# Kernel optimization log

Measured on AMD Instinct MI355X. Metric: run time of the kernel, lower is better.

The kernel has to match this reference:

```python
import jax, jax.numpy as jnp
import numpy as np

N, E, C, H = 100000, 3200000, 4, 64
EPS = 1e-8


def setup_inputs() -> dict:
    key = jax.random.key(0)
    k1, k2, k3, k4, k5, k6, k7 = jax.random.split(key, 7)
    x = jax.random.uniform(k1, (N, C), dtype=jnp.float32)            # [pm10, u10, v10, aux]
    pos = jax.random.normal(k2, (N, 2), dtype=jnp.float32)           # node coordinates
    edge_index = jax.random.randint(k3, (2, E), 0, N, dtype=jnp.int64)
    # PhysicsFluxLayer edge MLP: in = [x_i, x_j, wind_proj, dist] -> hidden
    fan_in = 2 * C + 2
    mlp_w = jax.random.normal(k4, (H, fan_in), dtype=jnp.float32) / np.sqrt(fan_in)
    mlp_b = jnp.zeros((H,), dtype=jnp.float32)
    # output head (module inits to zero; use small random values for a non-degenerate baseline)
    head_w = jax.random.normal(k5, (1, H), dtype=jnp.float32) * 0.02
    head_b = jax.random.normal(k6, (1,), dtype=jnp.float32) * 0.02
    return {"x": x, "pos": pos, "mlp_w": mlp_w, "mlp_b": mlp_b,
            "head_w": head_w, "head_b": head_b, "edge_index": edge_index}


def reference(x, pos, mlp_w, mlp_b, head_w, head_b, edge_index):
    src = edge_index[0]   # j (message source)
    dst = edge_index[1]   # i (message target)
    u10, v10 = x[:, 1], x[:, 2]
    # edge geometry: direction i -> j and distance
    d = pos[src] - pos[dst]                                  # [E,2]
    dist = jnp.sqrt(jnp.sum(d * d, axis=1) + EPS)            # [E]
    dhat = d / dist[:, None]
    # source wind projected onto the edge direction (advective transport term)
    wind_proj = u10[src] * dhat[:, 0] + v10[src] * dhat[:, 1]  # [E]
    edge_feat = jnp.concatenate(
        [x[dst], x[src], wind_proj[:, None], dist[:, None]], axis=1)  # [E, 2C+2]
    msg = jax.nn.relu(edge_feat @ mlp_w.T + mlp_b)            # [E,H]
    flux = jax.ops.segment_sum(msg, dst, num_segments=N)      # [N,H] scatter-add
    delta_pm10 = flux @ head_w.T + head_b                     # [N,1]
    pm10_next = jax.nn.softplus(x[:, 0:1] + delta_pm10)       # [N,1]
    return pm10_next, delta_pm10
```

## Files before the change

### kernel.cpp

```cpp
#include <hip/hip_runtime.h>
#include <hip/hip_bf16.h>


#define HID    64
#define EPSV   1e-8f
#define BNODES 256
#define CAP    10240
#define MAXB   512
#define BLK_SC 512
#define RPT_SC 24
#define LSTAGE (BLK_SC * RPT_SC)
#define BLK_C  256
#define SLOTW  20
#define OVF_CAP 65536

typedef _Float16 half8 __attribute__((ext_vector_type(8)));
typedef _Float16 half2_t __attribute__((ext_vector_type(2)));
typedef float f32x4 __attribute__((ext_vector_type(4)));

__device__ __forceinline__ unsigned int packh2(float a, float b) {
    union { half2_t h; unsigned int u; } v;
    v.h = half2_t{(_Float16)a, (_Float16)b};
    return v.u;
}

__device__ __forceinline__ void feat_from_rows(float4 xs, float4 ps4,
                                               float4 xd, float4 pd4,
                                               float* f) {
    float d0 = ps4.x - pd4.x;
    float d1 = ps4.y - pd4.y;
    float dist = sqrtf(fmaf(d0, d0, fmaf(d1, d1, EPSV)));
    float inv = 1.0f / dist;
    float wind = (xs.y * d0 + xs.z * d1) * inv;
    f[0] = xd.x; f[1] = xd.y; f[2] = xd.z; f[3] = xd.w;
    f[4] = xs.x; f[5] = xs.y; f[6] = xs.z; f[7] = xs.w;
    f[8] = wind; f[9] = dist;
}

__device__ __forceinline__ float mlp_scalar_g(const float* __restrict__ mlp_w,
                                              const float* __restrict__ mlp_b,
                                              const float* __restrict__ head_w,
                                              const float* f) {
    float sacc = 0.0f;
    for (int h = 0; h < HID; h++) {
        const float* wr = mlp_w + h * 10;
        float a = mlp_b[h];
        a = fmaf(wr[0], f[0], a); a = fmaf(wr[1], f[1], a);
        a = fmaf(wr[2], f[2], a); a = fmaf(wr[3], f[3], a);
        a = fmaf(wr[4], f[4], a); a = fmaf(wr[5], f[5], a);
        a = fmaf(wr[6], f[6], a); a = fmaf(wr[7], f[7], a);
        a = fmaf(wr[8], f[8], a); a = fmaf(wr[9], f[9], a);
        a = fmaxf(a, 0.0f);
        sacc = fmaf(head_w[h], a, sacc);
    }
    return sacc;
}

__global__ __launch_bounds__(BLK_SC, 4) void scatter_kernel(
    const int* __restrict__ srcs, const int* __restrict__ dsts,
    int E, int B, int N,
    const float4* __restrict__ x, const float2* __restrict__ pos,
    const float* __restrict__ mlp_w,
    float4* __restrict__ xpos, uint4* __restrict__ wbuf,
    unsigned long long* g_ptr64, unsigned int* __restrict__ sorted,
    int2* __restrict__ ovf, int* ovf_cnt)
{
    __shared__ int hist[MAXB];
    __shared__ int base[MAXB];
    __shared__ int pfx[MAXB];
    __shared__ int wsum[BLK_SC / 64];
    __shared__ unsigned int lpay[LSTAGE];
    __shared__ unsigned short lbid[LSTAGE];

    int tid  = threadIdx.x;
    int lane = tid & 63;
    int wid  = tid >> 6;
    int lo = blockIdx.x * LSTAGE;

    int es[RPT_SC], ed[RPT_SC];
    bool ev[RPT_SC];
    #pragma unroll
    for (int r = 0; r < RPT_SC; r++) {
        int e = lo + r * BLK_SC + tid;
        bool okr = (e < E);
        ev[r] = okr;
        int ee = okr ? e : 0;
        es[r] = srcs[ee];
        ed[r] = dsts[ee];
    }

    for (int b2 = tid; b2 < MAXB; b2 += BLK_SC) hist[b2] = 0;

    {
        int nper = (N + gridDim.x - 1) / gridDim.x;
        int n0 = blockIdx.x * nper;
        int n1 = min(n0 + nper, N);
        for (int n = n0 + tid; n < n1; n += BLK_SC) {
            float4 xr = x[n];
            float2 pr = pos[n];
            xpos[2 * n]     = xr;
            xpos[2 * n + 1] = make_float4(pr.x, pr.y, 0.0f, 0.0f);
        }
    }
    if (blockIdx.x == 0 && tid < 64) {
        int colw = tid & 15, quadw = tid >> 4;
        #pragma unroll
        for (int c = 0; c < 4; c++) {
            int h = c * 16 + colw;
            half8 wf = half8{0, 0, 0, 0, 0, 0, 0, 0};
            if (quadw == 0) {
                #pragma unroll
                for (int j = 0; j < 8; j++) wf[j] = (_Float16)mlp_w[h * 10 + j];
            } else if (quadw == 1) {
                wf[0] = (_Float16)mlp_w[h * 10 + 8];
                wf[1] = (_Float16)mlp_w[h * 10 + 9];
            }
            union { half8 h8; uint4 u4; } cv;
            cv.h8 = wf;
            wbuf[c * 64 + tid] = cv.u4;
        }
    }
    __syncthreads();

    #pragma unroll
    for (int r = 0; r < RPT_SC; r++) {
        if (ev[r]) {
            int b = ed[r] >> 8;
            int rk = atomicAdd(&hist[b], 1);
            es[r] = (es[r] << 8) | (ed[r] & 255);
            ed[r] = (b << 14) | rk;
        }
    }
    __syncthreads();

    int PB = (B + 1) >> 1;
    for (int p = tid; p < PB; p += BLK_SC) {
        int b0 = 2 * p, b1 = 2 * p + 1;
        unsigned long long h0 = (unsigned int)hist[b0];
        unsigned long long h1 = (b1 < B) ? (unsigned int)hist[b1] : 0ull;
        unsigned long long comb = h0 | (h1 << 32);
        unsigned long long old = 0ull;
        if (comb) old = atomicAdd(&g_ptr64[p], comb);
        base[b0] = (int)(old & 0xffffffffull);
        if (b1 < B) base[b1] = (int)(old >> 32);
    }
    int v = hist[tid];
    int xs_ = v;
    #pragma unroll
    for (int m = 1; m < 64; m <<= 1) {
        int y = __shfl_up(xs_, m, 64);
        if (lane >= m) xs_ += y;
    }
    if (lane == 63) wsum[wid] = xs_;
    __syncthreads();
    if (tid == 0) {
        int a = 0;
        #pragma unroll
        for (int j = 0; j < BLK_SC / 64; j++) { int t = wsum[j]; wsum[j] = a; a += t; }
    }
    __syncthreads();
    pfx[tid] = wsum[wid] + xs_ - v;
    __syncthreads();

    #pragma unroll
    for (int r = 0; r < RPT_SC; r++) {
        if (ev[r]) {
            int b  = ed[r] >> 14;
            int rk = ed[r] & 0x3FFF;
            int p  = pfx[b] + rk;
            lpay[p] = (unsigned int)es[r];
            lbid[p] = (unsigned short)b;
        }
    }
    __syncthreads();

    int cnt_blk = min(E - lo, LSTAGE);
    for (int t = tid; t < cnt_blk; t += BLK_SC) {
        unsigned int pay = lpay[t];
        int bid = (int)lbid[t];
        int rel = base[bid] + (t - pfx[bid]);
        if (rel < CAP) {
            sorted[(size_t)bid * CAP + rel] = pay;
        } else {
            int o = atomicAdd(ovf_cnt, 1);
            if (o < OVF_CAP)
                ovf[o] = make_int2((int)(pay >> 8), (bid << 8) | (int)(pay & 255u));
        }
    }
}

__global__ __launch_bounds__(BLK_C, 4) void compute_kernel(
    const float4* __restrict__ xpos,
    const uint4* __restrict__ wbuf,
    const float* __restrict__ mlp_w, const float* __restrict__ mlp_b,
    const float* __restrict__ head_w,
    const unsigned int* __restrict__ sorted,
    const unsigned long long* __restrict__ g_ptr64,
    const int2* __restrict__ ovf, const int* __restrict__ ovf_cnt,
    float* __restrict__ partial, int BB, int ksh, int N)
{
    __shared__ __align__(16) unsigned int stage[4 * 64 * SLOTW];
    __shared__ __align__(16) float4 drows[2 * BNODES];
    __shared__ float acc[BNODES];
    int tid  = threadIdx.x;
    int wave = tid >> 6;
    int lane = tid & 63;
    int col  = lane & 15;
    int quad = lane >> 4;
    int wbase = wave * 64 * SLOTW;

    int b    = blockIdx.x >> ksh;
    int part = blockIdx.x & ((1 << ksh) - 1);
    int nbase = b << 8;

    acc[tid] = 0.0f;

    {
        int lim = 2 * N - 1;
        drows[tid]       = xpos[min(2 * nbase + tid, lim)];
        drows[tid + 256] = xpos[min(2 * nbase + tid + 256, lim)];
    }

    {
        unsigned int* slotp = &stage[wbase + lane * SLOTW];
        slotp[5] = 0u;
        *(uint2*)(slotp + 6) = make_uint2(0u, 0u);
        *(uint4*)(slotp + 8) = make_uint4(0u, 0u, 0u, 0u);
        *(uint4*)(slotp + 12) = make_uint4(0u, 0u, 0u, 0u);
    }

    half8 wfr[4];
    f32x4 bias4[4], hw4[4];
    #pragma unroll
    for (int c = 0; c < 4; c++) {
        union { uint4 u4; half8 h8; } cv;
        cv.u4 = wbuf[c * 64 + lane];
        wfr[c] = cv.h8;
        bias4[c] = *(const f32x4*)&mlp_b[c * 16 + quad * 4];
        hw4[c]   = *(const f32x4*)&head_w[c * 16 + quad * 4];
    }
    __syncthreads();

    unsigned long long gp = g_ptr64[b >> 1];
    int cnt = (b & 1) ? (int)(gp >> 32) : (int)(gp & 0xffffffffull);
    cnt = min(cnt, CAP);
    int e0 = (cnt * part) >> ksh;
    int e1 = (cnt * (part + 1)) >> ksh;
    const unsigned int* sp = sorted + (size_t)b * CAP;

    if (e0 < e1) {
        unsigned int p0, p1, p2;
        float4 xA, pA, xB, pB, xC, pC;
        {
            int i = e0 + tid;
            p0 = sp[(i < e1) ? i : e0];
            int i1 = i + BLK_C;
            p1 = sp[(i1 < e1) ? i1 : e0];
            int s0 = (int)(p0 >> 8);
            xA = xpos[2 * s0];
            pA = xpos[2 * s0 + 1];
        }

        auto body = [&](int i0, unsigned int pc, unsigned int pn,
                        unsigned int& pn2, float4 xc, float4 psc,
                        float4& xn, float4& psn) {
            bool cok = (i0 + tid) < e1;
            int dl = (int)(pc & 255u);
            int i2 = i0 + 2 * BLK_C + tid;
            pn2 = sp[(i2 < e1) ? i2 : e0];
            int sn = (int)(pn >> 8);
            xn  = xpos[2 * sn];
            psn = xpos[2 * sn + 1];
            float4 xd  = drows[2 * dl];
            float4 pd4 = drows[2 * dl + 1];
            float f[10];
            feat_from_rows(xc, psc, xd, pd4, f);
            unsigned int* slotp = &stage[wbase + lane * SLOTW];
            *(uint4*)slotp = make_uint4(packh2(f[0], f[1]), packh2(f[2], f[3]),
                                        packh2(f[4], f[5]), packh2(f[6], f[7]));
            slotp[4] = packh2(f[8], f[9]);

            float mysum = 0.0f;
            #pragma unroll
            for (int eg = 0; eg < 4; eg++) {
                const half8 fb = *(const half8*)&stage[wbase + (eg * 16 + col) * SLOTW + quad * 4];
                float sacc = 0.0f;
                #pragma unroll
                for (int c = 0; c < 4; c++) {
                    f32x4 d = __builtin_amdgcn_mfma_f32_16x16x32_f16(wfr[c], fb, bias4[c], 0, 0, 0);
                    sacc = fmaf(hw4[c][0], fmaxf(d[0], 0.f), sacc);
                    sacc = fmaf(hw4[c][1], fmaxf(d[1], 0.f), sacc);
                    sacc = fmaf(hw4[c][2], fmaxf(d[2], 0.f), sacc);
                    sacc = fmaf(hw4[c][3], fmaxf(d[3], 0.f), sacc);
                }
                sacc += __shfl_xor(sacc, 16, 64);
                sacc += __shfl_xor(sacc, 32, 64);
                if (quad == eg) mysum = sacc;
            }
            if (cok) atomicAdd(&acc[dl], mysum);
        };

        int i0 = e0;
        for (;;) {
            body(i0, p0, p1, p2, xA, pA, xB, pB);
            i0 += BLK_C; if (i0 >= e1) break;
            body(i0, p1, p2, p0, xB, pB, xC, pC);
            i0 += BLK_C; if (i0 >= e1) break;
            body(i0, p2, p0, p1, xC, pC, xA, pA);
            i0 += BLK_C; if (i0 >= e1) break;
        }
    }
    __syncthreads();
    partial[(size_t)part * BB + nbase + tid] = acc[tid];

    if (part == 0) {
        __syncthreads();
        int oc = min(*ovf_cnt, OVF_CAP);
        for (int idx = tid; idx < oc; idx += BLK_C) {
            int2 sd = ovf[idx];
            if ((sd.y >> 8) == b) {
                float f[10];
                feat_from_rows(xpos[2 * sd.x], xpos[2 * sd.x + 1],
                               xpos[2 * sd.y], xpos[2 * sd.y + 1], f);
                unsafeAtomicAdd(&partial[sd.y], mlp_scalar_g(mlp_w, mlp_b, head_w, f));
            }
        }
    }
}

__global__ __launch_bounds__(512) void final_kernel(
    const float* __restrict__ xf,
    const float* __restrict__ partial, int BB,
    const float* __restrict__ head_b,
    float* __restrict__ out, int N, int kpart)
{
    int n = blockIdx.x * 512 + threadIdx.x;
    if (n >= N) return;
    float delta = head_b[0];
    for (int p = 0; p < kpart; p++)
        delta += partial[(size_t)p * BB + n];
    float v = xf[4 * n] + delta;
    float sp = fmaxf(v, 0.0f) + log1pf(expf(-fabsf(v)));
    out[n] = sp;
    out[N + n] = delta;
}

__global__ __launch_bounds__(256) void edge_kernel_fallback(
    const float4* __restrict__ x, const float2* __restrict__ pos,
    const float* __restrict__ mlp_w, const float* __restrict__ mlp_b,
    const float* __restrict__ head_w,
    const int* __restrict__ srcs, const int* __restrict__ dsts,
    float* __restrict__ delta_acc, int E)
{
    long e = (long)blockIdx.x * 256 + threadIdx.x;
    if (e >= E) return;
    int s = srcs[e], d = dsts[e];
    float4 xs = x[s], xd = x[d];
    float2 ps = pos[s], pd = pos[d];
    float f[10];
    feat_from_rows(xs, make_float4(ps.x, ps.y, 0, 0),
                   xd, make_float4(pd.x, pd.y, 0, 0), f);
    unsafeAtomicAdd(&delta_acc[d], mlp_scalar_g(mlp_w, mlp_b, head_w, f));
}

__global__ __launch_bounds__(256) void node_kernel_fallback(
    const float* __restrict__ xf, const float* __restrict__ delta_acc,
    const float* __restrict__ head_b, float* __restrict__ out, int N)
{
    int n = blockIdx.x * 256 + threadIdx.x;
    if (n >= N) return;
    float delta = delta_acc[n] + head_b[0];
    float v = xf[4 * n] + delta;
    float sp = fmaxf(v, 0.0f) + log1pf(expf(-fabsf(v)));
    out[n] = sp;
    out[N + n] = delta;
}

static inline size_t align_up(size_t v, size_t a) { return (v + a - 1) & ~(a - 1); }

extern "C" void kernel_launch(void* const* d_in, const int* in_sizes, int n_in,
                              void* d_out, int out_size, void* d_ws, size_t ws_size,
                              hipStream_t stream) {
    const float4* x      = (const float4*)d_in[0];
    const float2* pos    = (const float2*)d_in[1];
    const float*  mlp_w  = (const float*)d_in[2];
    const float*  mlp_b  = (const float*)d_in[3];
    const float*  head_w = (const float*)d_in[4];
    const float*  head_b = (const float*)d_in[5];
    const int*    ei     = (const int*)d_in[6];

    int N = in_sizes[0] / 4;
    int E = in_sizes[6] / 2;
    const int* srcs = ei;
    const int* dsts = ei + E;
    int B  = (N + BNODES - 1) / BNODES;
    int PB = (B + 1) >> 1;
    int BB = B * BNODES;

    size_t off = 0;
    unsigned long long* g_ptr64 = (unsigned long long*)((char*)d_ws + off);
    off = align_up(off + (size_t)PB * 8, 64);
    int* ovf_cnt = (int*)((char*)d_ws + off);
    size_t zero_bytes = off + 64;
    off = align_up(off + 64, 256);
    float4* xpos = (float4*)((char*)d_ws + off);
    off = align_up(off + (size_t)N * 32, 256);
    uint4* wbuf = (uint4*)((char*)d_ws + off);
    off = align_up(off + (size_t)4 * 64 * 16, 256);
    int2* ovf = (int2*)((char*)d_ws + off);
    off = align_up(off + (size_t)OVF_CAP * 8, 256);
    unsigned int* sorted = (unsigned int*)((char*)d_ws + off);
    off = align_up(off + (size_t)B * CAP * 4, 256);
    float* partial = (float*)((char*)d_ws + off);

    int kpart = 8, ksh = 3;
    if (off + (size_t)8 * BB * 4 > ws_size) { kpart = 4; ksh = 2; }
    size_t off_end = off + (size_t)kpart * BB * 4;
    bool fast = (off_end <= ws_size) && (B <= MAXB);

    if (fast) {
        hipMemsetAsync(d_ws, 0, zero_bytes, stream);
        int sgrid = (E + LSTAGE - 1) / LSTAGE;
        scatter_kernel<<<sgrid, BLK_SC, 0, stream>>>(
            srcs, dsts, E, B, N, x, pos, mlp_w,
            xpos, wbuf, g_ptr64, sorted, ovf, ovf_cnt);
        compute_kernel<<<B << ksh, BLK_C, 0, stream>>>(
            xpos, wbuf, mlp_w, mlp_b, head_w, sorted, g_ptr64,
            ovf, ovf_cnt, partial, BB, ksh, N);
        final_kernel<<<(N + 511) / 512, 512, 0, stream>>>(
            (const float*)x, partial, BB, head_b, (float*)d_out, N, kpart);
    } else {
        float* delta = (float*)d_ws;
        hipMemsetAsync(delta, 0, (size_t)N * sizeof(float), stream);
        edge_kernel_fallback<<<(int)((E + 255) / 256), 256, 0, stream>>>(
            x, pos, mlp_w, mlp_b, head_w, srcs, dsts, delta, E);
        node_kernel_fallback<<<(N + 255) / 256, 256, 0, stream>>>(
            (const float*)x, delta, head_b, (float*)d_out, N);
    }
}
```

Measured before the change: 146.0 us.

## Fuse scatter, compute and finalize into one cooperative persistent kernel

Replaces the memset plus three kernel launches with a single cooperative kernel that uses grid.sync between the bucketing, per-bucket MLP compute and softplus finalize phases. Shared memory is unioned across phases, blocks loop persistently over chunks and tasks, the compute phase grows to 512 threads, and the per-stage edge count and partition count shrink. The goal is to remove launch gaps and the memset. The cost is grid-wide barriers, a smaller resident grid than the old scatter and compute launches, and heavier register and shared-memory pressure that may limit occupancy.

```diff
diff --git a/kernel.cpp b/kernel.cpp
--- a/kernel.cpp
+++ b/kernel.cpp
@@ -1,5 +1,8 @@
 #include <hip/hip_runtime.h>
 #include <hip/hip_bf16.h>
+#include <hip/hip_cooperative_groups.h>
+
+namespace cg = cooperative_groups;
 
 
 #define HID    64
@@ -7,11 +10,12 @@
 #define BNODES 256
 #define CAP    10240
 #define MAXB   512
-#define BLK_SC 512
-#define RPT_SC 24
-#define LSTAGE (BLK_SC * RPT_SC)
-#define BLK_C  256
+#define BLKF   512
+#define RPTF   13
+#define LSTF   (BLKF * RPTF)
 #define SLOTW  20
+#define KPART  4
+#define KSH    2
 #define OVF_CAP 65536
 
 typedef _Float16 half8 __attribute__((ext_vector_type(8)));
@@ -56,173 +60,150 @@
     return sacc;
 }
 
-__global__ __launch_bounds__(BLK_SC, 4) void scatter_kernel(
+union FusedSh {
+    struct {
+        int hist[MAXB];
+        int base[MAXB];
+        int pfx[MAXB];
+        int wsum[BLKF / 64];
+        unsigned int   lpay[LSTF];
+        unsigned short lbid[LSTF];
+    } s;
+    struct {
+        unsigned int stage[8 * 64 * SLOTW];
+        float drows[2 * BNODES * 4];
+        float acc[BNODES];
+    } c;
+};
+
+__global__ __launch_bounds__(BLKF, 4) void fused_kernel(
+    const float4* __restrict__ x, const float2* __restrict__ pos,
+    const float* __restrict__ mlp_w, const float* __restrict__ mlp_b,
+    const float* __restrict__ head_w, const float* __restrict__ head_b,
     const int* __restrict__ srcs, const int* __restrict__ dsts,
-    int E, int B, int N,
-    const float4* __restrict__ x, const float2* __restrict__ pos,
-    const float* __restrict__ mlp_w,
-    float4* __restrict__ xpos, uint4* __restrict__ wbuf,
-    unsigned long long* g_ptr64, unsigned int* __restrict__ sorted,
-    int2* __restrict__ ovf, int* ovf_cnt)
+    float4* __restrict__ xpos,
+    unsigned long long* __restrict__ g_ptr64, int* __restrict__ ovf_cnt,
+    int2* __restrict__ ovf, unsigned int* __restrict__ sorted,
+    float* __restrict__ partial, float* __restrict__ out,
+    int N, int E, int B, int BB)
 {
-    __shared__ int hist[MAXB];
-    __shared__ int base[MAXB];
-    __shared__ int pfx[MAXB];
-    __shared__ int wsum[BLK_SC / 64];
-    __shared__ unsigned int lpay[LSTAGE];
-    __shared__ unsigned short lbid[LSTAGE];
+    __shared__ __align__(16) FusedSh sh;
+    cg::grid_group grid = cg::this_grid();
 
     int tid  = threadIdx.x;
+    int bid  = blockIdx.x;
+    int gsz  = gridDim.x;
     int lane = tid & 63;
     int wid  = tid >> 6;
-    int lo = blockIdx.x * LSTAGE;
-
-    int es[RPT_SC], ed[RPT_SC];
-    bool ev[RPT_SC];
-    #pragma unroll
-    for (int r = 0; r < RPT_SC; r++) {
-        int e = lo + r * BLK_SC + tid;
-        bool okr = (e < E);
-        ev[r] = okr;
-        int ee = okr ? e : 0;
-        es[r] = srcs[ee];
-        ed[r] = dsts[ee];
-    }
-
-    for (int b2 = tid; b2 < MAXB; b2 += BLK_SC) hist[b2] = 0;
-
-    {
-        int nper = (N + gridDim.x - 1) / gridDim.x;
-        int n0 = blockIdx.x * nper;
-        int n1 = min(n0 + nper, N);
-        for (int n = n0 + tid; n < n1; n += BLK_SC) {
-            float4 xr = x[n];
-            float2 pr = pos[n];
-            xpos[2 * n]     = xr;
-            xpos[2 * n + 1] = make_float4(pr.x, pr.y, 0.0f, 0.0f);
-        }
-    }
-    if (blockIdx.x == 0 && tid < 64) {
-        int colw = tid & 15, quadw = tid >> 4;
-        #pragma unroll
-        for (int c = 0; c < 4; c++) {
-            int h = c * 16 + colw;
-            half8 wf = half8{0, 0, 0, 0, 0, 0, 0, 0};
-            if (quadw == 0) {
-                #pragma unroll
-                for (int j = 0; j < 8; j++) wf[j] = (_Float16)mlp_w[h * 10 + j];
-            } else if (quadw == 1) {
-                wf[0] = (_Float16)mlp_w[h * 10 + 8];
-                wf[1] = (_Float16)mlp_w[h * 10 + 9];
-            }
-            union { half8 h8; uint4 u4; } cv;
-            cv.h8 = wf;
-            wbuf[c * 64 + tid] = cv.u4;
-        }
-    }
-    __syncthreads();
-
-    #pragma unroll
-    for (int r = 0; r < RPT_SC; r++) {
-        if (ev[r]) {
-            int b = ed[r] >> 8;
-            int rk = atomicAdd(&hist[b], 1);
-            es[r] = (es[r] << 8) | (ed[r] & 255);
-            ed[r] = (b << 14) | rk;
-        }
-    }
-    __syncthreads();
-
-    int PB = (B + 1) >> 1;
-    for (int p = tid; p < PB; p += BLK_SC) {
-        int b0 = 2 * p, b1 = 2 * p + 1;
-        unsigned long long h0 = (unsigned int)hist[b0];
-        unsigned long long h1 = (b1 < B) ? (unsigned int)hist[b1] : 0ull;
-        unsigned long long comb = h0 | (h1 << 32);
-        unsigned long long old = 0ull;
-        if (comb) old = atomicAdd(&g_ptr64[p], comb);
-        base[b0] = (int)(old & 0xffffffffull);
-        if (b1 < B) base[b1] = (int)(old >> 32);
-    }
-    int v = hist[tid];
-    int xs_ = v;
-    #pragma unroll
-    for (int m = 1; m < 64; m <<= 1) {
-        int y = __shfl_up(xs_, m, 64);
-        if (lane >= m) xs_ += y;
-    }
-    if (lane == 63) wsum[wid] = xs_;
-    __syncthreads();
-    if (tid == 0) {
-        int a = 0;
-        #pragma unroll
-        for (int j = 0; j < BLK_SC / 64; j++) { int t = wsum[j]; wsum[j] = a; a += t; }
-    }
-    __syncthreads();
-    pfx[tid] = wsum[wid] + xs_ - v;
-    __syncthreads();
-
-    #pragma unroll
-    for (int r = 0; r < RPT_SC; r++) {
-        if (ev[r]) {
-            int b  = ed[r] >> 14;
-            int rk = ed[r] & 0x3FFF;
-            int p  = pfx[b] + rk;
-            lpay[p] = (unsigned int)es[r];
-            lbid[p] = (unsigned short)b;
-        }
-    }
-    __syncthreads();
-
-    int cnt_blk = min(E - lo, LSTAGE);
-    for (int t = tid; t < cnt_blk; t += BLK_SC) {
-        unsigned int pay = lpay[t];
-        int bid = (int)lbid[t];
-        int rel = base[bid] + (t - pfx[bid]);
-        if (rel < CAP) {
-            sorted[(size_t)bid * CAP + rel] = pay;
-        } else {
-            int o = atomicAdd(ovf_cnt, 1);
-            if (o < OVF_CAP)
-                ovf[o] = make_int2((int)(pay >> 8), (bid << 8) | (int)(pay & 255u));
-        }
-    }
-}
-
-__global__ __launch_bounds__(BLK_C, 4) void compute_kernel(
-    const float4* __restrict__ xpos,
-    const uint4* __restrict__ wbuf,
-    const float* __restrict__ mlp_w, const float* __restrict__ mlp_b,
-    const float* __restrict__ head_w,
-    const unsigned int* __restrict__ sorted,
-    const unsigned long long* __restrict__ g_ptr64,
-    const int2* __restrict__ ovf, const int* __restrict__ ovf_cnt,
-    float* __restrict__ partial, int BB, int ksh, int N)
-{
-    __shared__ __align__(16) unsigned int stage[4 * 64 * SLOTW];
-    __shared__ __align__(16) float4 drows[2 * BNODES];
-    __shared__ float acc[BNODES];
-    int tid  = threadIdx.x;
-    int wave = tid >> 6;
-    int lane = tid & 63;
     int col  = lane & 15;
     int quad = lane >> 4;
-    int wbase = wave * 64 * SLOTW;
-
-    int b    = blockIdx.x >> ksh;
-    int part = blockIdx.x & ((1 << ksh) - 1);
-    int nbase = b << 8;
-
-    acc[tid] = 0.0f;
+
+    for (int n = bid * BLKF + tid; n < N; n += gsz * BLKF) {
+        float4 xr = x[n];
+        float2 pr = pos[n];
+        xpos[2 * n]     = xr;
+        xpos[2 * n + 1] = make_float4(pr.x, pr.y, 0.0f, 0.0f);
+    }
+    if (bid == 0) {
+        int PBv = (B + 1) >> 1;
+        for (int p = tid; p < PBv; p += BLKF) g_ptr64[p] = 0ull;
+        if (tid == 0) *ovf_cnt = 0;
+    }
+    grid.sync();
+
+    int nchunks = (E + LSTF - 1) / LSTF;
+    for (int chunk = bid; chunk < nchunks; chunk += gsz) {
+        int lo = chunk * LSTF;
+
+        int es[RPTF], ed[RPTF];
+        bool ev[RPTF];
+        #pragma unroll
+        for (int r = 0; r < RPTF; r++) {
+            int e = lo + r * BLKF + tid;
+            bool okr = (e < E);
+            ev[r] = okr;
+            int ee = okr ? e : 0;
+            es[r] = srcs[ee];
+            ed[r] = dsts[ee];
+        }
+
+        sh.s.hist[tid] = 0;
+        __syncthreads();
+
+        #pragma unroll
+        for (int r = 0; r < RPTF; r++) {
+            if (ev[r]) {
+                int b = ed[r] >> 8;
+                int rk = atomicAdd(&sh.s.hist[b], 1);
+                es[r] = (es[r] << 8) | (ed[r] & 255);
+                ed[r] = (b << 14) | rk;
+            }
+        }
+        __syncthreads();
+
+        int PBv = (B + 1) >> 1;
+        for (int p = tid; p < PBv; p += BLKF) {
+            int b0 = 2 * p, b1 = 2 * p + 1;
+            unsigned long long h0 = (unsigned int)sh.s.hist[b0];
+            unsigned long long h1 = (b1 < B) ? (unsigned int)sh.s.hist[b1] : 0ull;
+            unsigned long long comb = h0 | (h1 << 32);
+            unsigned long long old = 0ull;
+            if (comb) old = atomicAdd(&g_ptr64[p], comb);
+            sh.s.base[b0] = (int)(old & 0xffffffffull);
+            if (b1 < B) sh.s.base[b1] = (int)(old >> 32);
+        }
+        int v = sh.s.hist[tid];
+        int xs_ = v;
+        #pragma unroll
+        for (int m = 1; m < 64; m <<= 1) {
+            int y = __shfl_up(xs_, m, 64);
+            if (lane >= m) xs_ += y;
+        }
+        if (lane == 63) sh.s.wsum[wid] = xs_;
+        __syncthreads();
+        if (tid == 0) {
+            int a = 0;
+            #pragma unroll
+            for (int j = 0; j < BLKF / 64; j++) { int t = sh.s.wsum[j]; sh.s.wsum[j] = a; a += t; }
+        }
+        __syncthreads();
+        sh.s.pfx[tid] = sh.s.wsum[wid] + xs_ - v;
+        __syncthreads();
+
+        #pragma unroll
+        for (int r = 0; r < RPTF; r++) {
+            if (ev[r]) {
+                int b  = ed[r] >> 14;
+                int rk = ed[r] & 0x3FFF;
+                int p  = sh.s.pfx[b] + rk;
+                sh.s.lpay[p] = (unsigned int)es[r];
+                sh.s.lbid[p] = (unsigned short)b;
+            }
+        }
+        __syncthreads();
+
+        int cnt_blk = min(E - lo, LSTF);
+        for (int t = tid; t < cnt_blk; t += BLKF) {
+            unsigned int pay = sh.s.lpay[t];
+            int bidb = (int)sh.s.lbid[t];
+            int rel = sh.s.base[bidb] + (t - sh.s.pfx[bidb]);
+            if (rel < CAP) {
+                sorted[(size_t)bidb * CAP + rel] = pay;
+            } else {
+                int o = atomicAdd(ovf_cnt, 1);
+                if (o < OVF_CAP)
+                    ovf[o] = make_int2((int)(pay >> 8), (bidb << 8) | (int)(pay & 255u));
+            }
+        }
+        __syncthreads();
+    }
+    grid.sync();
+
+    float4* drows = (float4*)sh.c.drows;
+    int wbase = wid * 64 * SLOTW;
 
     {
-        int lim = 2 * N - 1;
-        drows[tid]       = xpos[min(2 * nbase + tid, lim)];
-        drows[tid + 256] = xpos[min(2 * nbase + tid + 256, lim)];
-    }
-
-    {
-        unsigned int* slotp = &stage[wbase + lane * SLOTW];
+        unsigned int* slotp = &sh.c.stage[wbase + lane * SLOTW];
         slotp[5] = 0u;
         *(uint2*)(slotp + 6) = make_uint2(0u, 0u);
         *(uint4*)(slotp + 8) = make_uint4(0u, 0u, 0u, 0u);
@@ -233,116 +214,133 @@
     f32x4 bias4[4], hw4[4];
     #pragma unroll
     for (int c = 0; c < 4; c++) {
-        union { uint4 u4; half8 h8; } cv;
-        cv.u4 = wbuf[c * 64 + lane];
-        wfr[c] = cv.h8;
+        int h = c * 16 + col;
+        half8 wf = half8{0, 0, 0, 0, 0, 0, 0, 0};
+        if (quad == 0) {
+            #pragma unroll
+            for (int j = 0; j < 8; j++) wf[j] = (_Float16)mlp_w[h * 10 + j];
+        } else if (quad == 1) {
+            wf[0] = (_Float16)mlp_w[h * 10 + 8];
+            wf[1] = (_Float16)mlp_w[h * 10 + 9];
+        }
+        wfr[c] = wf;
         bias4[c] = *(const f32x4*)&mlp_b[c * 16 + quad * 4];
         hw4[c]   = *(const f32x4*)&head_w[c * 16 + quad * 4];
     }
-    __syncthreads();
-
-    unsigned long long gp = g_ptr64[b >> 1];
-    int cnt = (b & 1) ? (int)(gp >> 32) : (int)(gp & 0xffffffffull);
-    cnt = min(cnt, CAP);
-    int e0 = (cnt * part) >> ksh;
-    int e1 = (cnt * (part + 1)) >> ksh;
-    const unsigned int* sp = sorted + (size_t)b * CAP;
-
-    if (e0 < e1) {
-        unsigned int p0, p1, p2;
-        float4 xA, pA, xB, pB, xC, pC;
+
+    int ntask = B * KPART;
+    for (int task = bid; task < ntask; task += gsz) {
+        int b    = task >> KSH;
+        int part = task & (KPART - 1);
+        int nbase = b << 8;
+
+        if (tid < BNODES) sh.c.acc[tid] = 0.0f;
         {
-            int i = e0 + tid;
-            p0 = sp[(i < e1) ? i : e0];
-            int i1 = i + BLK_C;
-            p1 = sp[(i1 < e1) ? i1 : e0];
-            int s0 = (int)(p0 >> 8);
-            xA = xpos[2 * s0];
-            pA = xpos[2 * s0 + 1];
-        }
-
-        auto body = [&](int i0, unsigned int pc, unsigned int pn,
-                        unsigned int& pn2, float4 xc, float4 psc,
-                        float4& xn, float4& psn) {
-            bool cok = (i0 + tid) < e1;
-            int dl = (int)(pc & 255u);
-            int i2 = i0 + 2 * BLK_C + tid;
-            pn2 = sp[(i2 < e1) ? i2 : e0];
-            int sn = (int)(pn >> 8);
-            xn  = xpos[2 * sn];
-            psn = xpos[2 * sn + 1];
-            float4 xd  = drows[2 * dl];
-            float4 pd4 = drows[2 * dl + 1];
-            float f[10];
-            feat_from_rows(xc, psc, xd, pd4, f);
-            unsigned int* slotp = &stage[wbase + lane * SLOTW];
-            *(uint4*)slotp = make_uint4(packh2(f[0], f[1]), packh2(f[2], f[3]),
-                                        packh2(f[4], f[5]), packh2(f[6], f[7]));
-            slotp[4] = packh2(f[8], f[9]);
-
-            float mysum = 0.0f;
-            #pragma unroll
-            for (int eg = 0; eg < 4; eg++) {
-                const half8 fb = *(const half8*)&stage[wbase + (eg * 16 + col) * SLOTW + quad * 4];
-                float sacc = 0.0f;
+            int lim = 2 * N - 1;
+            drows[tid] = xpos[min(2 * nbase + tid, lim)];
+        }
+        __syncthreads();
+
+        unsigned long long gp = g_ptr64[b >> 1];
+        int cnt = (b & 1) ? (int)(gp >> 32) : (int)(gp & 0xffffffffull);
+        cnt = min(cnt, CAP);
+        int e0 = (cnt * part) >> KSH;
+        int e1 = (cnt * (part + 1)) >> KSH;
+        const unsigned int* sp = sorted + (size_t)b * CAP;
+
+        if (e0 < e1) {
+            unsigned int p0, p1, p2;
+            float4 xA, pA, xB, pB, xC, pC;
+            {
+                int i = e0 + tid;
+                p0 = sp[(i < e1) ? i : e0];
+                int i1 = i + BLKF;
+                p1 = sp[(i1 < e1) ? i1 : e0];
+                int s0 = (int)(p0 >> 8);
+                xA = xpos[2 * s0];
+                pA = xpos[2 * s0 + 1];
+            }
+
+            auto body = [&](int i0, unsigned int pc, unsigned int pn,
+                            unsigned int& pn2, float4 xc, float4 psc,
+                            float4& xn, float4& psn) {
+                bool cok = (i0 + tid) < e1;
+                int dl = (int)(pc & 255u);
+                int i2 = i0 + 2 * BLKF + tid;
+                pn2 = sp[(i2 < e1) ? i2 : e0];
+                int sn = (int)(pn >> 8);
+                xn  = xpos[2 * sn];
+                psn = xpos[2 * sn + 1];
+                float4 xd  = drows[2 * dl];
+                float4 pd4 = drows[2 * dl + 1];
+                float f[10];
+                feat_from_rows(xc, psc, xd, pd4, f);
+                unsigned int* slotp = &sh.c.stage[wbase + lane * SLOTW];
+                *(uint4*)slotp = make_uint4(packh2(f[0], f[1]), packh2(f[2], f[3]),
+                                            packh2(f[4], f[5]), packh2(f[6], f[7]));
+                slotp[4] = packh2(f[8], f[9]);
+
+                float mysum = 0.0f;
                 #pragma unroll
-                for (int c = 0; c < 4; c++) {
-                    f32x4 d = __builtin_amdgcn_mfma_f32_16x16x32_f16(wfr[c], fb, bias4[c], 0, 0, 0);
-                    sacc = fmaf(hw4[c][0], fmaxf(d[0], 0.f), sacc);
-                    sacc = fmaf(hw4[c][1], fmaxf(d[1], 0.f), sacc);
-                    sacc = fmaf(hw4[c][2], fmaxf(d[2], 0.f), sacc);
-                    sacc = fmaf(hw4[c][3], fmaxf(d[3], 0.f), sacc);
+                for (int eg = 0; eg < 4; eg++) {
+                    const half8 fb = *(const half8*)&sh.c.stage[wbase + (eg * 16 + col) * SLOTW + quad * 4];
+                    float sacc = 0.0f;
+                    #pragma unroll
+                    for (int c = 0; c < 4; c++) {
+                        f32x4 d = __builtin_amdgcn_mfma_f32_16x16x32_f16(wfr[c], fb, bias4[c], 0, 0, 0);
+                        sacc = fmaf(hw4[c][0], fmaxf(d[0], 0.f), sacc);
+                        sacc = fmaf(hw4[c][1], fmaxf(d[1], 0.f), sacc);
+                        sacc = fmaf(hw4[c][2], fmaxf(d[2], 0.f), sacc);
+                        sacc = fmaf(hw4[c][3], fmaxf(d[3], 0.f), sacc);
+                    }
+                    sacc += __shfl_xor(sacc, 16, 64);
+                    sacc += __shfl_xor(sacc, 32, 64);
+                    if (quad == eg) mysum = sacc;
                 }
-                sacc += __shfl_xor(sacc, 16, 64);
-                sacc += __shfl_xor(sacc, 32, 64);
-                if (quad == eg) mysum = sacc;
-            }
-            if (cok) atomicAdd(&acc[dl], mysum);
-        };
-
-        int i0 = e0;
-        for (;;) {
-            body(i0, p0, p1, p2, xA, pA, xB, pB);
-            i0 += BLK_C; if (i0 >= e1) break;
-            body(i0, p1, p2, p0, xB, pB, xC, pC);
-            i0 += BLK_C; if (i0 >= e1) break;
-            body(i0, p2, p0, p1, xC, pC, xA, pA);
-            i0 += BLK_C; if (i0 >= e1) break;
-        }
-    }
-    __syncthreads();
-    partial[(size_t)part * BB + nbase + tid] = acc[tid];
-
-    if (part == 0) {
-        __syncthreads();
-        int oc = min(*ovf_cnt, OVF_CAP);
-        for (int idx = tid; idx < oc; idx += BLK_C) {
-            int2 sd = ovf[idx];
-            if ((sd.y >> 8) == b) {
-                float f[10];
-                feat_from_rows(xpos[2 * sd.x], xpos[2 * sd.x + 1],
-                               xpos[2 * sd.y], xpos[2 * sd.y + 1], f);
-                unsafeAtomicAdd(&partial[sd.y], mlp_scalar_g(mlp_w, mlp_b, head_w, f));
-            }
-        }
-    }
-}
-
-__global__ __launch_bounds__(512) void final_kernel(
-    const float* __restrict__ xf,
-    const float* __restrict__ partial, int BB,
-    const float* __restrict__ head_b,
-    float* __restrict__ out, int N, int kpart)
-{
-    int n = blockIdx.x * 512 + threadIdx.x;
-    if (n >= N) return;
-    float delta = head_b[0];
-    for (int p = 0; p < kpart; p++)
-        delta += partial[(size_t)p * BB + n];
-    float v = xf[4 * n] + delta;
-    float sp = fmaxf(v, 0.0f) + log1pf(expf(-fabsf(v)));
-    out[n] = sp;
-    out[N + n] = delta;
+                if (cok) atomicAdd(&sh.c.acc[dl], mysum);
+            };
+
+            int i0 = e0;
+            for (;;) {
+                body(i0, p0, p1, p2, xA, pA, xB, pB);
+                i0 += BLKF; if (i0 >= e1) break;
+                body(i0, p1, p2, p0, xB, pB, xC, pC);
+                i0 += BLKF; if (i0 >= e1) break;
+                body(i0, p2, p0, p1, xC, pC, xA, pA);
+                i0 += BLKF; if (i0 >= e1) break;
+            }
+        }
+        __syncthreads();
+        if (tid < BNODES) partial[(size_t)part * BB + nbase + tid] = sh.c.acc[tid];
+
+        if (part == 0) {
+            __syncthreads();
+            int oc = min(*ovf_cnt, OVF_CAP);
+            for (int idx = tid; idx < oc; idx += BLKF) {
+                int2 sd = ovf[idx];
+                if ((sd.y >> 8) == b) {
+                    float f[10];
+                    feat_from_rows(xpos[2 * sd.x], xpos[2 * sd.x + 1],
+                                   xpos[2 * sd.y], xpos[2 * sd.y + 1], f);
+                    unsafeAtomicAdd(&partial[sd.y], mlp_scalar_g(mlp_w, mlp_b, head_w, f));
+                }
+            }
+        }
+        __syncthreads();
+    }
+    grid.sync();
+
+    const float* xf = (const float*)x;
+    for (int n = bid * BLKF + tid; n < N; n += gsz * BLKF) {
+        float delta = head_b[0];
+        #pragma unroll
+        for (int p = 0; p < KPART; p++)
+            delta += partial[(size_t)p * BB + n];
+        float v = xf[4 * n] + delta;
+        float sp = fmaxf(v, 0.0f) + log1pf(expf(-fabsf(v)));
+        out[n] = sp;
+        out[N + n] = delta;
+    }
 }
 
 __global__ __launch_bounds__(256) void edge_kernel_fallback(
@@ -401,34 +399,48 @@
     unsigned long long* g_ptr64 = (unsigned long long*)((char*)d_ws + off);
     off = align_up(off + (size_t)PB * 8, 64);
     int* ovf_cnt = (int*)((char*)d_ws + off);
-    size_t zero_bytes = off + 64;
     off = align_up(off + 64, 256);
     float4* xpos = (float4*)((char*)d_ws + off);
     off = align_up(off + (size_t)N * 32, 256);
-    uint4* wbuf = (uint4*)((char*)d_ws + off);
-    off = align_up(off + (size_t)4 * 64 * 16, 256);
     int2* ovf = (int2*)((char*)d_ws + off);
     off = align_up(off + (size_t)OVF_CAP * 8, 256);
     unsigned int* sorted = (unsigned int*)((char*)d_ws + off);
     off = align_up(off + (size_t)B * CAP * 4, 256);
     float* partial = (float*)((char*)d_ws + off);
-
-    int kpart = 8, ksh = 3;
-    if (off + (size_t)8 * BB * 4 > ws_size) { kpart = 4; ksh = 2; }
-    size_t off_end = off + (size_t)kpart * BB * 4;
-    bool fast = (off_end <= ws_size) && (B <= MAXB);
+    size_t off_end = off + (size_t)KPART * BB * 4;
+
+    static int coopState = -1;
+    static int coopGrid  = 0;
+    if (coopState < 0) {
+        int dev = 0;
+        hipGetDevice(&dev);
+        int cl = 0, ncu = 0, mb = 0;
+        hipDeviceGetAttribute(&cl, hipDeviceAttributeCooperativeLaunch, dev);
+        hipDeviceGetAttribute(&ncu, hipDeviceAttributeMultiprocessorCount, dev);
+        hipError_t oe = hipOccupancyMaxActiveBlocksPerMultiprocessor(
+            &mb, fused_kernel, BLKF, 0);
+        if (cl && oe == hipSuccess && mb > 0 && ncu > 0) {
+            coopState = 1;
+            coopGrid  = mb * ncu;
+        } else {
+            coopState = 0;
+        }
+    }
+
+    bool fast = (coopState == 1) && (off_end <= ws_size) && (B <= MAXB)
+                && (coopGrid >= 8);
 
     if (fast) {
-        hipMemsetAsync(d_ws, 0, zero_bytes, stream);
-        int sgrid = (E + LSTAGE - 1) / LSTAGE;
-        scatter_kernel<<<sgrid, BLK_SC, 0, stream>>>(
-            srcs, dsts, E, B, N, x, pos, mlp_w,
-            xpos, wbuf, g_ptr64, sorted, ovf, ovf_cnt);
-        compute_kernel<<<B << ksh, BLK_C, 0, stream>>>(
-            xpos, wbuf, mlp_w, mlp_b, head_w, sorted, g_ptr64,
-            ovf, ovf_cnt, partial, BB, ksh, N);
-        final_kernel<<<(N + 511) / 512, 512, 0, stream>>>(
-            (const float*)x, partial, BB, head_b, (float*)d_out, N, kpart);
+        float* outp = (float*)d_out;
+        void* args[] = {
+            (void*)&x, (void*)&pos, (void*)&mlp_w, (void*)&mlp_b,
+            (void*)&head_w, (void*)&head_b, (void*)&srcs, (void*)&dsts,
+            (void*)&xpos, (void*)&g_ptr64, (void*)&ovf_cnt, (void*)&ovf,
+            (void*)&sorted, (void*)&partial, (void*)&outp,
+            (void*)&N, (void*)&E, (void*)&B, (void*)&BB
+        };
+        hipLaunchCooperativeKernel((void*)fused_kernel, dim3(coopGrid),
+                                   dim3(BLKF), args, 0, stream);
     } else {
         float* delta = (float*)d_ws;
         hipMemsetAsync(delta, 0, (size_t)N * sizeof(float), stream);
```

Result: slower. 263.5 us (+80.5%).
